# Performance work log

Measured on AMD Instinct MI355X. Metric: run time of the kernel, lower is better.

## Reference

```python
import jax, jax.numpy as jnp
import numpy as np

ATT_HEAD, IN_DIM, OUT_DIM = 4, 256, 64
LEAKY_ALPHA = 0.2
B, N_SRC, N_DST = 4, 2048, 2048


def setup_inputs() -> dict:
    key = jax.random.key(0)
    ks = jax.random.split(key, 8)
    def xavier(k, shape, fan_in, fan_out):
        lim = float(np.sqrt(6.0 / (fan_in + fan_out)))
        return jax.random.uniform(k, shape, jnp.float32, -lim, lim)
    feat_src = jax.random.normal(ks[0], (B, N_SRC, IN_DIM), jnp.float32)
    feat_dst = jax.random.normal(ks[1], (B, N_DST, IN_DIM), jnp.float32)
    W = xavier(ks[2], (ATT_HEAD, IN_DIM, OUT_DIM), IN_DIM, OUT_DIM)
    b = jnp.zeros((OUT_DIM,), jnp.float32)
    w_src = xavier(ks[3], (ATT_HEAD, OUT_DIM), OUT_DIM, 1)
    w_dst = xavier(ks[4], (ATT_HEAD, OUT_DIM), OUT_DIM, 1)
    # nn.Linear(in_dim, in_dim) with xavier_normal_ weight, default-init bias
    std = float(np.sqrt(2.0 / (IN_DIM + IN_DIM)))
    H_w = jax.random.normal(ks[5], (IN_DIM, IN_DIM), jnp.float32) * std
    lim_b = float(1.0 / np.sqrt(IN_DIM))
    H_b = jax.random.uniform(ks[6], (IN_DIM,), jnp.float32, -lim_b, lim_b)
    return {"feat_src": feat_src, "feat_dst": feat_dst, "W": W, "b": b,
            "w_src": w_src, "w_dst": w_dst, "H_w": H_w, "H_b": H_b}


def reference(feat_src, feat_dst, W, b, w_src, w_dst, H_w, H_b):
    # Projections: [B, H, N, out_dim]
    h_src = jnp.einsum('bni,hio->bhno', feat_src, W)
    h_dst = jnp.einsum('bmi,hio->bhmo', feat_dst, W)
    # Additive attention logits
    a_src = jnp.einsum('bhno,ho->bhn', jnp.tanh(h_src), w_src)  # [B,H,N_src]
    a_dst = jnp.einsum('bhmo,ho->bhm', jnp.tanh(h_dst), w_dst)  # [B,H,N_dst]
    attn = a_src[..., :, None] + a_dst[..., None, :]            # [B,H,N_src,N_dst]
    attn = jax.nn.leaky_relu(attn, LEAKY_ALPHA)
    attn = jax.nn.softmax(attn, axis=-1)
    # Weighted sum over dst nodes
    feat_out = jnp.einsum('bhnm,bhmo->bhno', attn, h_dst) + b   # [B,H,N_src,out]
    B_, H_, N_, O_ = feat_out.shape
    feat_out = jnp.transpose(feat_out, (0, 2, 1, 3)).reshape(B_, N_, H_ * O_)
    feat_out = jax.nn.elu(feat_out)
    gate = jax.nn.sigmoid(feat_src @ H_w.T + H_b)
    out = gate * feat_out + (1.0 - gate) * feat_src
    # dropout is identity in eval mode
    return out
```

## Files before the change

### kernel.cpp

```cpp
#include <hip/hip_runtime.h>
#include <math.h>

typedef unsigned int uint32;
typedef __attribute__((ext_vector_type(8))) short bf16x8;
typedef __attribute__((ext_vector_type(4))) float f32x4;

#define BB 4
#define HH 4
#define NSRC 2048
#define NDST 2048
#define IND 256
#define OUTD 64
#define ALPHA 0.2f
#define NB 2048
#define NCH 256

#define OFF_HDST   0
#define OFF_ASRC   2097152
#define OFF_ADST   2129920
#define OFF_PK     2162688
#define OFF_C1     2293760
#define OFF_C2     2555904
#define OFF_CZ1    2818048
#define OFF_CZ2    2822144
#define OFF_T1     2826240
#define OFF_TZ1    2827264
#define OFF_TZ2    2827280
#define OFF_BST    2827296
#define OFF_MM     2860080
#define OFF_GFH    2860112
#define OFF_GFL    2892880

__device__ __forceinline__ float fast_tanh(float x) {
    float e = __expf(2.f * x);
    return 1.f - 2.f / (e + 1.f);
}

__device__ __forceinline__ uint32 f32_to_bf16_rne(float x) {
    uint32 u = __float_as_uint(x);
    return (u + 0x7fffu + ((u >> 16) & 1u)) >> 16;
}

__device__ __forceinline__ void split8(const float* x, bf16x8& h8, bf16x8& l8) {
    uint32 hw[4], lw[4];
    #pragma unroll
    for (int p = 0; p < 4; ++p) {
        uint32 h0 = f32_to_bf16_rne(x[2 * p]);
        float f0 = __uint_as_float(h0 << 16);
        uint32 l0 = f32_to_bf16_rne(x[2 * p] - f0);
        uint32 h1 = f32_to_bf16_rne(x[2 * p + 1]);
        float f1 = __uint_as_float(h1 << 16);
        uint32 l1 = f32_to_bf16_rne(x[2 * p + 1] - f1);
        hw[p] = h0 | (h1 << 16);
        lw[p] = l0 | (l1 << 16);
    }
    h8 = *(bf16x8*)hw; l8 = *(bf16x8*)lw;
}

__global__ __launch_bounds__(256) void k1_mfma(const float* __restrict__ feat_src,
                                               const float* __restrict__ feat_dst,
                                               const float* __restrict__ W,
                                               const float* __restrict__ w_src,
                                               const float* __restrict__ w_dst,
                                               float* __restrict__ ws) {
    __shared__ __align__(16) unsigned short Ahi[32 * 256];
    __shared__ __align__(16) unsigned short Alo[32 * 256];
    int bid = blockIdx.x;
    int t = bid & 63, b = (bid >> 6) & 3, s = bid >> 8;
    int tid = threadIdx.x;
    const float* feat = s ? feat_dst : feat_src;
    const float4* fb = (const float4*)(feat + ((size_t)b * 2048 + t * 32) * IND);
    #pragma unroll
    for (int it = 0; it < 8; ++it) {
        int f4 = it * 256 + tid;
        int row = f4 >> 6, c4 = f4 & 63;
        float4 v = fb[f4];
        float xs[4] = {v.x, v.y, v.z, v.w};
        uint32 hb[4], lb[4];
        #pragma unroll
        for (int j = 0; j < 4; ++j) {
            hb[j] = f32_to_bf16_rne(xs[j]);
            float hf = __uint_as_float(hb[j] << 16);
            lb[j] = f32_to_bf16_rne(xs[j] - hf);
        }
        uint2 hw, lw;
        hw.x = hb[0] | (hb[1] << 16); hw.y = hb[2] | (hb[3] << 16);
        lw.x = lb[0] | (lb[1] << 16); lw.y = lb[2] | (lb[3] << 16);
        int baddr = (row * 512 + c4 * 8) ^ ((row & 7) << 4);
        *(uint2*)((char*)Ahi + baddr) = hw;
        *(uint2*)((char*)Alo + baddr) = lw;
    }
    __syncthreads();
    int w = tid >> 6, l = tid & 63;
    int lr = l & 15, lq = l >> 4;
    const float* Wh = W + (size_t)w * 16384;
    f32x4 acc[2][4];
    #pragma unroll
    for (int mi = 0; mi < 2; ++mi)
        #pragma unroll
        for (int ni = 0; ni < 4; ++ni) acc[mi][ni] = (f32x4)0.f;
    for (int ks = 0; ks < 8; ++ks) {
        bf16x8 ah[2], al[2], bh8[4], bl8[4];
        #pragma unroll
        for (int mi = 0; mi < 2; ++mi) {
            int row = mi * 16 + lr;
            int baddr = (row * 512 + ks * 64 + lq * 16) ^ ((row & 7) << 4);
            ah[mi] = *(const bf16x8*)((const char*)Ahi + baddr);
            al[mi] = *(const bf16x8*)((const char*)Alo + baddr);
        }
        int kb = ks * 32 + lq * 8;
        #pragma unroll
        for (int ni = 0; ni < 4; ++ni) {
            const float* wp = Wh + (size_t)kb * 64 + ni * 16 + lr;
            float xv[8];
            #pragma unroll
            for (int j = 0; j < 8; ++j) xv[j] = wp[j * 64];
            split8(xv, bh8[ni], bl8[ni]);
        }
        #pragma unroll
        for (int mi = 0; mi < 2; ++mi)
            #pragma unroll
            for (int ni = 0; ni < 4; ++ni) {
                acc[mi][ni] = __builtin_amdgcn_mfma_f32_16x16x32_bf16(ah[mi], bh8[ni], acc[mi][ni], 0, 0, 0);
                acc[mi][ni] = __builtin_amdgcn_mfma_f32_16x16x32_bf16(ah[mi], bl8[ni], acc[mi][ni], 0, 0, 0);
                acc[mi][ni] = __builtin_amdgcn_mfma_f32_16x16x32_bf16(al[mi], bh8[ni], acc[mi][ni], 0, 0, 0);
            }
    }
    if (s) {
        float* hd = ws + OFF_HDST + ((size_t)(b * HH + w) * NDST + t * 32) * OUTD;
        #pragma unroll
        for (int mi = 0; mi < 2; ++mi)
            #pragma unroll
            for (int ni = 0; ni < 4; ++ni)
                #pragma unroll
                for (int r = 0; r < 4; ++r)
                    hd[(mi * 16 + lq * 4 + r) * 64 + ni * 16 + lr] = acc[mi][ni][r];
    }
    const float* wa = (s ? w_dst : w_src) + w * OUTD;
    float wa_v[4];
    #pragma unroll
    for (int ni = 0; ni < 4; ++ni) wa_v[ni] = wa[ni * 16 + lr];
    float* ap = ws + (s ? OFF_ADST : OFF_ASRC) + (b * HH + w) * NSRC + t * 32;
    #pragma unroll
    for (int mi = 0; mi < 2; ++mi)
        #pragma unroll
        for (int r = 0; r < 4; ++r) {
            float p = 0.f;
            #pragma unroll
            for (int ni = 0; ni < 4; ++ni) p += fast_tanh(acc[mi][ni][r]) * wa_v[ni];
            p += __shfl_xor(p, 1); p += __shfl_xor(p, 2);
            p += __shfl_xor(p, 4); p += __shfl_xor(p, 8);
            if (lr == 0) ap[mi * 16 + lq * 4 + r] = p;
        }
}

__global__ __launch_bounds__(1024) void kmid(const float* __restrict__ Hw,
                                             float* __restrict__ ws) {
    if (blockIdx.x >= 16) {
        int g = (blockIdx.x - 16) * 1024 + threadIdx.x;
        int l = g & 63, ni = (g >> 6) & 3, ks = (g >> 8) & 7, cb = g >> 11;
        int col = cb * 64 + ni * 16 + (l & 15);
        int k0 = ks * 32 + (l >> 4) * 8;
        unsigned short hs[8], lsv[8];
        #pragma unroll
        for (int j = 0; j < 8; ++j) {
            float w = Hw[(size_t)col * 256 + k0 + j];
            uint32 hb = f32_to_bf16_rne(w);
            float hf = __uint_as_float(hb << 16);
            uint32 lb = f32_to_bf16_rne(w - hf);
            hs[j] = (unsigned short)hb; lsv[j] = (unsigned short)lb;
        }
        unsigned short* fh = (unsigned short*)(ws + OFF_GFH);
        unsigned short* fl = (unsigned short*)(ws + OFF_GFL);
        int slab = ((cb * 8 + ks) * 4 + ni) * 512 + l * 8;
        #pragma unroll
        for (int j = 0; j < 8; ++j) { fh[slab + j] = hs[j]; fl[slab + j] = lsv[j]; }
        return;
    }
    __shared__ int   hist[2048];
    __shared__ float keysP[2048];
    __shared__ int   idxP[2048];
    __shared__ float w1L[2048];
    __shared__ float w2L[2048];
    __shared__ float ST1[16 * 64], ST2[16 * 64];
    __shared__ float SZ1[16], SZ2[16];
    __shared__ float red[32];
    __shared__ float loinv[2];
    __shared__ int wtot[16];
    int bh = blockIdx.x, tid = threadIdx.x;
    int lane = tid & 63, wv = tid >> 6;
    const float* ad = ws + OFF_ADST + bh * NDST;
    float d0 = ad[tid], d1 = ad[tid + 1024];
    float mn = fminf(d0, d1), mx = fmaxf(d0, d1);
    #pragma unroll
    for (int off = 32; off; off >>= 1) {
        mn = fminf(mn, __shfl_xor(mn, off));
        mx = fmaxf(mx, __shfl_xor(mx, off));
    }
    if (lane == 0) { red[wv] = mn; red[16 + wv] = mx; }
    hist[tid] = 0; hist[tid + 1024] = 0;
    __syncthreads();
    if (tid == 0) {
        float lo = red[0], hi = red[16];
        #pragma unroll
        for (int i = 1; i < 16; ++i) { lo = fminf(lo, red[i]); hi = fmaxf(hi, red[16 + i]); }
        float wd = hi - lo;
        float inv = (float)NB / (wd + wd * 1e-6f + 1e-30f);
        loinv[0] = lo; loinv[1] = inv;
        ws[OFF_MM + bh * 2] = lo; ws[OFF_MM + bh * 2 + 1] = inv;
    }
    __syncthreads();
    float lo = loinv[0], inv = loinv[1];
    int b0 = (int)((d0 - lo) * inv); b0 = b0 < 0 ? 0 : (b0 > NB - 1 ? NB - 1 : b0);
    int b1 = (int)((d1 - lo) * inv); b1 = b1 < 0 ? 0 : (b1 > NB - 1 ? NB - 1 : b1);
    atomicAdd(&hist[b0], 1);
    atomicAdd(&hist[b1], 1);
    __syncthreads();
    int h0 = hist[2 * tid], h1 = hist[2 * tid + 1];
    int s = h0 + h1, sc = s;
    #pragma unroll
    for (int off = 1; off < 64; off <<= 1) {
        int v = __shfl_up(sc, off);
        if (lane >= off) sc += v;
    }
    if (lane == 63) wtot[wv] = sc;
    __syncthreads();
    if (tid == 0) {
        int r = 0;
        #pragma unroll
        for (int i = 0; i < 16; ++i) { int v = wtot[i]; wtot[i] = r; r += v; }
    }
    __syncthreads();
    int base = wtot[wv] + (sc - s);
    int* bstg = (int*)(ws + OFF_BST) + bh * (NB + 1);
    hist[2 * tid] = base;
    hist[2 * tid + 1] = base + h0;
    bstg[2 * tid] = base;
    bstg[2 * tid + 1] = base + h0;
    if (tid == 0) bstg[NB] = NDST;
    __syncthreads();
    int p0 = atomicAdd(&hist[b0], 1);
    keysP[p0] = d0; idxP[p0] = tid;
    w1L[p0] = __expf(d0); w2L[p0] = __expf(ALPHA * d0);
    int p1 = atomicAdd(&hist[b1], 1);
    keysP[p1] = d1; idxP[p1] = tid + 1024;
    w1L[p1] = __expf(d1); w2L[p1] = __expf(ALPHA * d1);
    __syncthreads();
    {
        float4* pkg = (float4*)(ws + OFF_PK) + (size_t)bh * 2048;
        pkg[tid] = make_float4(keysP[tid], w1L[tid], w2L[tid],
                               __int_as_float(idxP[tid] * 64));
        pkg[tid + 1024] = make_float4(keysP[tid + 1024], w1L[tid + 1024], w2L[tid + 1024],
                                      __int_as_float(idxP[tid + 1024] * 64));
    }
    const float* hd = ws + OFF_HDST + (size_t)bh * NDST * OUTD;
    float* C1g = ws + OFF_C1 + (size_t)bh * NCH * 64;
    float* C2g = ws + OFF_C2 + (size_t)bh * NCH * 64;
    float* CZ1g = ws + OFF_CZ1 + bh * NCH;
    float* CZ2g = ws + OFF_CZ2 + bh * NCH;
    int o = lane;
    float run1 = 0.f, run2 = 0.f, rz1 = 0.f, rz2 = 0.f;
    for (int k = 0; k < 16; ++k) {
        int c = wv * 16 + k;
        float c1 = 0.f, c2 = 0.f, cz1 = 0.f, cz2 = 0.f;
        #pragma unroll
        for (int ii = 0; ii < 8; ++ii) {
            int i = c * 8 + ii;
            int m = idxP[i];
            float w1 = w1L[i], w2 = w2L[i];
            float hv = hd[m * 64 + o];
            c1 += w1 * hv; c2 += w2 * hv; cz1 += w1; cz2 += w2;
        }
        C1g[c * 64 + o] = c1; C2g[c * 64 + o] = c2;
        if (o == 0) { CZ1g[c] = cz1; CZ2g[c] = cz2; }
        run1 += c1; run2 += c2; rz1 += cz1; rz2 += cz2;
    }
    ST1[wv * 64 + o] = run1; ST2[wv * 64 + o] = run2;
    if (lane == 0) { SZ1[wv] = rz1; SZ2[wv] = rz2; }
    __syncthreads();
    float base1 = 0.f, base2 = 0.f, zb1 = 0.f, zb2 = 0.f;
    for (int ss = 0; ss < wv; ++ss) {
        base1 += ST1[ss * 64 + o]; base2 += ST2[ss * 64 + o];
        zb1 += SZ1[ss];            zb2 += SZ2[ss];
    }
    if (wv == 15) {
        ws[OFF_T1 + bh * 64 + o] = base1 + run1;
        if (o == 0) { ws[OFF_TZ1 + bh] = zb1 + rz1; ws[OFF_TZ2 + bh] = zb2 + rz2; }
    }
    float a1 = base1, a2 = base2, az1 = zb1, az2 = zb2;
    for (int k = 0; k < 16; ++k) {
        int c = wv * 16 + k;
        float v1 = C1g[c * 64 + o]; C1g[c * 64 + o] = a1; a1 += v1;
        float v2 = C2g[c * 64 + o]; C2g[c * 64 + o] = a2; a2 += v2;
        if (o == 0) {
            float vz1 = CZ1g[c]; CZ1g[c] = az1; az1 += vz1;
            float vz2 = CZ2g[c]; CZ2g[c] = az2; az2 += vz2;
        }
    }
}

#define FSTR 260
__global__ __launch_bounds__(512) void k34(const float* __restrict__ feat_src,
                                           const float* __restrict__ Hb,
                                           const float* __restrict__ bias,
                                           const float* __restrict__ ws,
                                           float* __restrict__ out) {
    __shared__ float FOUT[16 * FSTR];
    __shared__ __align__(16) unsigned short Ahi[16 * 256];
    __shared__ __align__(16) unsigned short Alo[16 * 256];
    int bid = blockIdx.x;
    int b = bid >> 7, brow = (bid & 127) * 16;
    int tid = threadIdx.x;
    int o = tid & 63;
    int wv = __builtin_amdgcn_readfirstlane(tid >> 6);
    const float4* fb = (const float4*)(feat_src + ((size_t)b * 2048 + brow) * IND);
    #pragma unroll
    for (int it = 0; it < 2; ++it) {
        int f4 = it * 512 + tid;
        int row = f4 >> 6, c4 = f4 & 63;
        float4 v = fb[f4];
        float xs[4] = {v.x, v.y, v.z, v.w};
        uint32 hb[4], lb[4];
        #pragma unroll
        for (int j = 0; j < 4; ++j) {
            hb[j] = f32_to_bf16_rne(xs[j]);
            float hf = __uint_as_float(hb[j] << 16);
            lb[j] = f32_to_bf16_rne(xs[j] - hf);
        }
        uint2 hw, lw;
        hw.x = hb[0] | (hb[1] << 16); hw.y = hb[2] | (hb[3] << 16);
        lw.x = lb[0] | (lb[1] << 16); lw.y = lb[2] | (lb[3] << 16);
        int baddr = (row * 512 + c4 * 8) ^ ((row & 7) << 4);
        *(uint2*)((char*)Ahi + baddr) = hw;
        *(uint2*)((char*)Alo + baddr) = lw;
    }
    {
        int h = wv >> 1;
        int bh = b * 4 + h;
        int nbase = (wv & 1) * 8;
        float T1v = ws[OFF_T1 + bh * 64 + o];
        float tz1 = ws[OFF_TZ1 + bh], tz2 = ws[OFF_TZ2 + bh];
        float blo = ws[OFF_MM + bh * 2], binv = ws[OFF_MM + bh * 2 + 1];
        float biasv = bias[o];
        int r_l = o & 7;
        float t_l = ws[OFF_ASRC + bh * 2048 + brow + nbase + r_l];
        float th_l = -t_l;
        int bk = (int)floorf((th_l - blo) * binv);
        bk = bk < 0 ? 0 : (bk > NB - 1 ? NB - 1 : bk);
        const int* bst = (const int*)(ws + OFF_BST) + bh * (NB + 1);
        int jstart = bst[bk], jend = bst[bk + 1];
        int cch = (jstart + 4) >> 3; if (cch > NCH - 1) cch = NCH - 1;
        int i0c_l = cch << 3;
        int lo2_l = i0c_l < jstart ? i0c_l : jstart;
        int hi2_l = i0c_l > jend ? i0c_l : jend;
        float czp1_l = ws[OFF_CZ1 + bh * NCH + cch];
        float czp2_l = ws[OFF_CZ2 + bh * NCH + cch];
        float c1v[8], c2v[8];
        #pragma unroll
        for (int r = 0; r < 8; ++r) {
            int cch_r = __builtin_amdgcn_readfirstlane(__shfl(cch, r));
            c1v[r] = ws[OFF_C1 + ((size_t)bh * NCH + cch_r) * 64 + o];
            c2v[r] = ws[OFF_C2 + ((size_t)bh * NCH + cch_r) * 64 + o];
        }
        const float4* pk = (const float4*)(ws + OFF_PK) + (size_t)bh * 2048;
        const float* hd = ws + OFF_HDST + (size_t)bh * NDST * OUTD;
        #pragma unroll
        for (int r = 0; r < 8; ++r) {
            float t_r = __uint_as_float(
                __builtin_amdgcn_readfirstlane(__float_as_uint(__shfl(t_l, r))));
            float th = -t_r;
            int i0c = __builtin_amdgcn_readfirstlane(__shfl(i0c_l, r));
            int lo2 = __builtin_amdgcn_readfirstlane(__shfl(lo2_l, r));
            int hi2 = __builtin_amdgcn_readfirstlane(__shfl(hi2_l, r));
            float p1 = c1v[r], p2 = c2v[r];
            float zp1 = __shfl(czp1_l, r), zp2 = __shfl(czp2_l, r);
            for (int i = lo2; i < hi2; i += 8) {
                float4 q[8];
                #pragma unroll
                for (int j = 0; j < 8; ++j) {
                    int ii = i + j < hi2 ? i + j : hi2 - 1;
                    q[j] = pk[ii];
                }
                float hv[8];
                #pragma unroll
                for (int j = 0; j < 8; ++j)
                    hv[j] = hd[__float_as_int(q[j].w) + o];
                #pragma unroll
                for (int j = 0; j < 8; ++j) {
                    float sel = (q[j].x <= th ? 1.f : 0.f) - (i + j < i0c ? 1.f : 0.f);
                    sel = (i + j < hi2) ? sel : 0.f;
                    float w1 = q[j].y * sel, w2 = q[j].z * sel;
                    p1 += w1 * hv[j]; p2 += w2 * hv[j]; zp1 += w1; zp2 += w2;
                }
            }
            float et = __expf(t_r), et2 = __expf(ALPHA * t_r);
            float num = et * (T1v - p1) + et2 * p2;
            float den = et * (tz1 - zp1) + et2 * zp2;
            FOUT[(nbase + r) * FSTR + h * 64 + o] = num / den + biasv;
        }
    }
    __syncthreads();
    int l = tid & 63;
    int lr = l & 15, lq = l >> 4;
    int cb = wv >> 1, nb = (wv & 1) * 2;
    const uint4* gfh = (const uint4*)(ws + OFF_GFH);
    const uint4* gfl = (const uint4*)(ws + OFF_GFL);
    f32x4 acc[2];
    acc[0] = (f32x4)0.f; acc[1] = (f32x4)0.f;
    for (int ks = 0; ks < 8; ++ks) {
        bf16x8 ah, al, bh8[2], bl8[2];
        {
            int row = lr;
            int baddr = (row * 512 + ks * 64 + lq * 16) ^ ((row & 7) << 4);
            ah = *(const bf16x8*)((const char*)Ahi + baddr);
            al = *(const bf16x8*)((const char*)Alo + baddr);
        }
        #pragma unroll
        for (int ni = 0; ni < 2; ++ni) {
            int idx = ((cb * 8 + ks) * 4 + nb + ni) * 64 + l;
            uint4 th_ = gfh[idx], tl_ = gfl[idx];
            bh8[ni] = *(const bf16x8*)&th_;
            bl8[ni] = *(const bf16x8*)&tl_;
        }
        #pragma unroll
        for (int ni = 0; ni < 2; ++ni) {
            acc[ni] = __builtin_amdgcn_mfma_f32_16x16x32_bf16(ah, bh8[ni], acc[ni], 0, 0, 0);
            acc[ni] = __builtin_amdgcn_mfma_f32_16x16x32_bf16(ah, bl8[ni], acc[ni], 0, 0, 0);
            acc[ni] = __builtin_amdgcn_mfma_f32_16x16x32_bf16(al, bh8[ni], acc[ni], 0, 0, 0);
        }
    }
    #pragma unroll
    for (int ni = 0; ni < 2; ++ni) {
        int c = cb * 64 + (nb + ni) * 16 + lr;
        float hbv = Hb[c];
        #pragma unroll
        for (int r = 0; r < 4; ++r) {
            int rl = lq * 4 + r;
            size_t rg = (size_t)b * 2048 + brow + rl;
            float x = acc[ni][r] + hbv;
            float g = 1.f / (1.f + __expf(-x));
            float fo = FOUT[rl * FSTR + c];
            float e = fo > 0.f ? fo : expm1f(fo);
            float fs = feat_src[rg * 256 + c];
            out[rg * 256 + c] = g * e + (1.f - g) * fs;
        }
    }
}

extern "C" void kernel_launch(void* const* d_in, const int* in_sizes, int n_in,
                              void* d_out, int out_size, void* d_ws, size_t ws_size,
                              hipStream_t stream) {
    const float* feat_src = (const float*)d_in[0];
    const float* feat_dst = (const float*)d_in[1];
    const float* W        = (const float*)d_in[2];
    const float* bias     = (const float*)d_in[3];
    const float* w_src    = (const float*)d_in[4];
    const float* w_dst    = (const float*)d_in[5];
    const float* Hw       = (const float*)d_in[6];
    const float* Hb       = (const float*)d_in[7];
    float* out = (float*)d_out;
    float* ws  = (float*)d_ws;

    k1_mfma<<<512, 256, 0, stream>>>(feat_src, feat_dst, W, w_src, w_dst, ws);
    kmid<<<24, 1024, 0, stream>>>(Hw, ws);
    k34<<<512, 512, 0, stream>>>(feat_src, Hb, bias, ws, out);
}
```

Baseline: 66.96 us.

## Fuse three kernels into one persistent cooperative kernel with grid syncs

Replaces the three separate launches (projection, dst sort/prefix, output+gate) with a single cooperative persistent kernel. Phases are separated by grid-wide syncs, and blocks loop over tiles. The projection phase now uses 512-thread blocks that split output columns across wave halves and reduce partial logits through shared memory. The intent is to remove launch gaps and inter-kernel drain. In exchange, the middle phase runs on only 24 blocks while the rest of the grid waits at the barrier, and occupancy is capped by the cooperative launch.

Measured after the change: 248.2 us. 3.71x slower.

```diff
diff --git a/kernel.cpp b/kernel.cpp
--- a/kernel.cpp
+++ b/kernel.cpp
@@ -1,5 +1,8 @@
 #include <hip/hip_runtime.h>
+#include <hip/hip_cooperative_groups.h>
 #include <math.h>
+
+namespace cg = cooperative_groups;
 
 typedef unsigned int uint32;
 typedef __attribute__((ext_vector_type(8))) short bf16x8;
@@ -57,392 +60,442 @@
     h8 = *(bf16x8*)hw; l8 = *(bf16x8*)lw;
 }
 
-__global__ __launch_bounds__(256) void k1_mfma(const float* __restrict__ feat_src,
-                                               const float* __restrict__ feat_dst,
-                                               const float* __restrict__ W,
-                                               const float* __restrict__ w_src,
-                                               const float* __restrict__ w_dst,
-                                               float* __restrict__ ws) {
-    __shared__ __align__(16) unsigned short Ahi[32 * 256];
-    __shared__ __align__(16) unsigned short Alo[32 * 256];
-    int bid = blockIdx.x;
-    int t = bid & 63, b = (bid >> 6) & 3, s = bid >> 8;
-    int tid = threadIdx.x;
-    const float* feat = s ? feat_dst : feat_src;
-    const float4* fb = (const float4*)(feat + ((size_t)b * 2048 + t * 32) * IND);
-    #pragma unroll
-    for (int it = 0; it < 8; ++it) {
-        int f4 = it * 256 + tid;
-        int row = f4 >> 6, c4 = f4 & 63;
-        float4 v = fb[f4];
-        float xs[4] = {v.x, v.y, v.z, v.w};
-        uint32 hb[4], lb[4];
+#define FSTR 260
+#define SMEM_BYTES 45312
+
+__global__ __launch_bounds__(512, 4) void fused_all(
+        const float* __restrict__ feat_src, const float* __restrict__ feat_dst,
+        const float* __restrict__ W, const float* __restrict__ w_src,
+        const float* __restrict__ w_dst, const float* __restrict__ Hw,
+        const float* __restrict__ Hb, const float* __restrict__ bias,
+        float* __restrict__ ws, float* __restrict__ out) {
+    cg::grid_group gg = cg::this_grid();
+    __shared__ __align__(16) char smem[SMEM_BYTES];
+    const int tid = threadIdx.x;
+    const int nblk = gridDim.x;
+    const int lane = tid & 63, wv = tid >> 6;
+
+    {
+        unsigned short* Ahi = (unsigned short*)smem;
+        unsigned short* Alo = (unsigned short*)(smem + 16384);
+        float* APART = (float*)(smem + 32768);
+        int hh = wv & 3, half = wv >> 2, nb = half * 2;
+        int lr = lane & 15, lq = lane >> 4;
+        const float* Wh = W + (size_t)hh * 16384;
+        for (int tile = blockIdx.x; tile < 512; tile += nblk) {
+            __syncthreads();
+            int t = tile & 63, b = (tile >> 6) & 3, s = tile >> 8;
+            const float* feat = s ? feat_dst : feat_src;
+            const float4* fb = (const float4*)(feat + ((size_t)b * 2048 + t * 32) * IND);
+            #pragma unroll
+            for (int it = 0; it < 4; ++it) {
+                int f4 = it * 512 + tid;
+                int row = f4 >> 6, c4 = f4 & 63;
+                float4 v = fb[f4];
+                float xs[4] = {v.x, v.y, v.z, v.w};
+                uint32 hb[4], lb[4];
+                #pragma unroll
+                for (int j = 0; j < 4; ++j) {
+                    hb[j] = f32_to_bf16_rne(xs[j]);
+                    float hf = __uint_as_float(hb[j] << 16);
+                    lb[j] = f32_to_bf16_rne(xs[j] - hf);
+                }
+                uint2 hw, lw;
+                hw.x = hb[0] | (hb[1] << 16); hw.y = hb[2] | (hb[3] << 16);
+                lw.x = lb[0] | (lb[1] << 16); lw.y = lb[2] | (lb[3] << 16);
+                int baddr = (row * 512 + c4 * 8) ^ ((row & 7) << 4);
+                *(uint2*)((char*)Ahi + baddr) = hw;
+                *(uint2*)((char*)Alo + baddr) = lw;
+            }
+            __syncthreads();
+            f32x4 acc[2][2];
+            #pragma unroll
+            for (int mi = 0; mi < 2; ++mi)
+                #pragma unroll
+                for (int ni = 0; ni < 2; ++ni) acc[mi][ni] = (f32x4)0.f;
+            for (int ks = 0; ks < 8; ++ks) {
+                bf16x8 ah[2], al[2], bh8[2], bl8[2];
+                #pragma unroll
+                for (int mi = 0; mi < 2; ++mi) {
+                    int row = mi * 16 + lr;
+                    int baddr = (row * 512 + ks * 64 + lq * 16) ^ ((row & 7) << 4);
+                    ah[mi] = *(const bf16x8*)((const char*)Ahi + baddr);
+                    al[mi] = *(const bf16x8*)((const char*)Alo + baddr);
+                }
+                int kb = ks * 32 + lq * 8;
+                #pragma unroll
+                for (int ni = 0; ni < 2; ++ni) {
+                    const float* wp = Wh + (size_t)kb * 64 + (nb + ni) * 16 + lr;
+                    float xv[8];
+                    #pragma unroll
+                    for (int j = 0; j < 8; ++j) xv[j] = wp[j * 64];
+                    split8(xv, bh8[ni], bl8[ni]);
+                }
+                #pragma unroll
+                for (int mi = 0; mi < 2; ++mi)
+                    #pragma unroll
+                    for (int ni = 0; ni < 2; ++ni) {
+                        acc[mi][ni] = __builtin_amdgcn_mfma_f32_16x16x32_bf16(ah[mi], bh8[ni], acc[mi][ni], 0, 0, 0);
+                        acc[mi][ni] = __builtin_amdgcn_mfma_f32_16x16x32_bf16(ah[mi], bl8[ni], acc[mi][ni], 0, 0, 0);
+                        acc[mi][ni] = __builtin_amdgcn_mfma_f32_16x16x32_bf16(al[mi], bh8[ni], acc[mi][ni], 0, 0, 0);
+                    }
+            }
+            if (s) {
+                float* hd = ws + OFF_HDST + ((size_t)(b * HH + hh) * NDST + t * 32) * OUTD;
+                #pragma unroll
+                for (int mi = 0; mi < 2; ++mi)
+                    #pragma unroll
+                    for (int ni = 0; ni < 2; ++ni)
+                        #pragma unroll
+                        for (int r = 0; r < 4; ++r)
+                            hd[(mi * 16 + lq * 4 + r) * 64 + (nb + ni) * 16 + lr] = acc[mi][ni][r];
+            }
+            const float* wa = (s ? w_dst : w_src) + hh * OUTD;
+            float wa_v[2];
+            #pragma unroll
+            for (int ni = 0; ni < 2; ++ni) wa_v[ni] = wa[(nb + ni) * 16 + lr];
+            #pragma unroll
+            for (int mi = 0; mi < 2; ++mi)
+                #pragma unroll
+                for (int r = 0; r < 4; ++r) {
+                    float p = fast_tanh(acc[mi][0][r]) * wa_v[0]
+                            + fast_tanh(acc[mi][1][r]) * wa_v[1];
+                    p += __shfl_xor(p, 1); p += __shfl_xor(p, 2);
+                    p += __shfl_xor(p, 4); p += __shfl_xor(p, 8);
+                    if (lr == 0) APART[half * 128 + hh * 32 + mi * 16 + lq * 4 + r] = p;
+                }
+            __syncthreads();
+            if (tid < 128) {
+                int hh2 = tid >> 5, row = tid & 31;
+                float a = APART[hh2 * 32 + row] + APART[128 + hh2 * 32 + row];
+                ws[(s ? OFF_ADST : OFF_ASRC) + (b * HH + hh2) * NSRC + t * 32 + row] = a;
+            }
+        }
+    }
+    __threadfence();
+    gg.sync();
+
+    for (int wb = blockIdx.x; wb < 24; wb += nblk) {
+        __syncthreads();
+        if (wb >= 16) {
+            #pragma unroll
+            for (int q = 0; q < 2; ++q) {
+                int g = (wb - 16) * 1024 + q * 512 + tid;
+                int l = g & 63, ni = (g >> 6) & 3, ks = (g >> 8) & 7, cb = g >> 11;
+                int col = cb * 64 + ni * 16 + (l & 15);
+                int k0 = ks * 32 + (l >> 4) * 8;
+                unsigned short hs[8], lsv[8];
+                #pragma unroll
+                for (int j = 0; j < 8; ++j) {
+                    float w = Hw[(size_t)col * 256 + k0 + j];
+                    uint32 hb = f32_to_bf16_rne(w);
+                    float hf = __uint_as_float(hb << 16);
+                    uint32 lb = f32_to_bf16_rne(w - hf);
+                    hs[j] = (unsigned short)hb; lsv[j] = (unsigned short)lb;
+                }
+                unsigned short* fh = (unsigned short*)(ws + OFF_GFH);
+                unsigned short* fl = (unsigned short*)(ws + OFF_GFL);
+                int slab = ((cb * 8 + ks) * 4 + ni) * 512 + l * 8;
+                #pragma unroll
+                for (int j = 0; j < 8; ++j) { fh[slab + j] = hs[j]; fl[slab + j] = lsv[j]; }
+            }
+            continue;
+        }
+        int bh = wb;
+        int* hist = (int*)smem;
+        float* keysP = (float*)(smem + 8192);
+        int* idxP = (int*)(smem + 16384);
+        float* w1L = (float*)(smem + 24576);
+        float* w2L = (float*)(smem + 32768);
+        float* ST1 = (float*)(smem + 40960);
+        float* ST2 = (float*)(smem + 43008);
+        float* SZ1 = (float*)(smem + 45056);
+        float* SZ2 = (float*)(smem + 45088);
+        float* red = (float*)(smem + 45120);
+        float* loinv = (float*)(smem + 45184);
+        int* wtot = (int*)(smem + 45192);
+        const float* ad = ws + OFF_ADST + bh * NDST;
+        float d0 = ad[tid], d1 = ad[tid + 512], d2 = ad[tid + 1024], d3 = ad[tid + 1536];
+        float mn = fminf(fminf(d0, d1), fminf(d2, d3));
+        float mx = fmaxf(fmaxf(d0, d1), fmaxf(d2, d3));
         #pragma unroll
-        for (int j = 0; j < 4; ++j) {
-            hb[j] = f32_to_bf16_rne(xs[j]);
-            float hf = __uint_as_float(hb[j] << 16);
-            lb[j] = f32_to_bf16_rne(xs[j] - hf);
-        }
-        uint2 hw, lw;
-        hw.x = hb[0] | (hb[1] << 16); hw.y = hb[2] | (hb[3] << 16);
-        lw.x = lb[0] | (lb[1] << 16); lw.y = lb[2] | (lb[3] << 16);
-        int baddr = (row * 512 + c4 * 8) ^ ((row & 7) << 4);
-        *(uint2*)((char*)Ahi + baddr) = hw;
-        *(uint2*)((char*)Alo + baddr) = lw;
+        for (int off = 32; off; off >>= 1) {
+            mn = fminf(mn, __shfl_xor(mn, off));
+            mx = fmaxf(mx, __shfl_xor(mx, off));
+        }
+        if (lane == 0) { red[wv] = mn; red[8 + wv] = mx; }
+        hist[tid] = 0; hist[tid + 512] = 0; hist[tid + 1024] = 0; hist[tid + 1536] = 0;
+        __syncthreads();
+        if (tid == 0) {
+            float lo = red[0], hi = red[8];
+            #pragma unroll
+            for (int i = 1; i < 8; ++i) { lo = fminf(lo, red[i]); hi = fmaxf(hi, red[8 + i]); }
+            float wd = hi - lo;
+            float inv = (float)NB / (wd + wd * 1e-6f + 1e-30f);
+            loinv[0] = lo; loinv[1] = inv;
+            ws[OFF_MM + bh * 2] = lo; ws[OFF_MM + bh * 2 + 1] = inv;
+        }
+        __syncthreads();
+        float lo = loinv[0], inv = loinv[1];
+        int bk0 = (int)((d0 - lo) * inv); bk0 = bk0 < 0 ? 0 : (bk0 > NB - 1 ? NB - 1 : bk0);
+        int bk1 = (int)((d1 - lo) * inv); bk1 = bk1 < 0 ? 0 : (bk1 > NB - 1 ? NB - 1 : bk1);
+        int bk2 = (int)((d2 - lo) * inv); bk2 = bk2 < 0 ? 0 : (bk2 > NB - 1 ? NB - 1 : bk2);
+        int bk3 = (int)((d3 - lo) * inv); bk3 = bk3 < 0 ? 0 : (bk3 > NB - 1 ? NB - 1 : bk3);
+        atomicAdd(&hist[bk0], 1); atomicAdd(&hist[bk1], 1);
+        atomicAdd(&hist[bk2], 1); atomicAdd(&hist[bk3], 1);
+        __syncthreads();
+        int h0 = hist[4 * tid], h1 = hist[4 * tid + 1], h2 = hist[4 * tid + 2], h3 = hist[4 * tid + 3];
+        int s = h0 + h1 + h2 + h3, sc = s;
+        #pragma unroll
+        for (int off = 1; off < 64; off <<= 1) {
+            int v = __shfl_up(sc, off);
+            if (lane >= off) sc += v;
+        }
+        if (lane == 63) wtot[wv] = sc;
+        __syncthreads();
+        if (tid == 0) {
+            int r = 0;
+            #pragma unroll
+            for (int i = 0; i < 8; ++i) { int v = wtot[i]; wtot[i] = r; r += v; }
+        }
+        __syncthreads();
+        int base = wtot[wv] + (sc - s);
+        int* bstg = (int*)(ws + OFF_BST) + bh * (NB + 1);
+        hist[4 * tid] = base;                    bstg[4 * tid] = base;
+        hist[4 * tid + 1] = base + h0;           bstg[4 * tid + 1] = base + h0;
+        hist[4 * tid + 2] = base + h0 + h1;      bstg[4 * tid + 2] = base + h0 + h1;
+        hist[4 * tid + 3] = base + h0 + h1 + h2; bstg[4 * tid + 3] = base + h0 + h1 + h2;
+        if (tid == 0) bstg[NB] = NDST;
+        __syncthreads();
+        {
+            int p = atomicAdd(&hist[bk0], 1);
+            keysP[p] = d0; idxP[p] = tid;
+            w1L[p] = __expf(d0); w2L[p] = __expf(ALPHA * d0);
+            p = atomicAdd(&hist[bk1], 1);
+            keysP[p] = d1; idxP[p] = tid + 512;
+            w1L[p] = __expf(d1); w2L[p] = __expf(ALPHA * d1);
+            p = atomicAdd(&hist[bk2], 1);
+            keysP[p] = d2; idxP[p] = tid + 1024;
+            w1L[p] = __expf(d2); w2L[p] = __expf(ALPHA * d2);
+            p = atomicAdd(&hist[bk3], 1);
+            keysP[p] = d3; idxP[p] = tid + 1536;
+            w1L[p] = __expf(d3); w2L[p] = __expf(ALPHA * d3);
+        }
+        __syncthreads();
+        {
+            float4* pkg = (float4*)(ws + OFF_PK) + (size_t)bh * 2048;
+            #pragma unroll
+            for (int j = 0; j < 4; ++j) {
+                int i = tid + j * 512;
+                pkg[i] = make_float4(keysP[i], w1L[i], w2L[i], __int_as_float(idxP[i] * 64));
+            }
+        }
+        const float* hd = ws + OFF_HDST + (size_t)bh * NDST * OUTD;
+        float* C1g = ws + OFF_C1 + (size_t)bh * NCH * 64;
+        float* C2g = ws + OFF_C2 + (size_t)bh * NCH * 64;
+        float* CZ1g = ws + OFF_CZ1 + bh * NCH;
+        float* CZ2g = ws + OFF_CZ2 + bh * NCH;
+        int o = lane;
+        float run1 = 0.f, run2 = 0.f, rz1 = 0.f, rz2 = 0.f;
+        for (int k = 0; k < 32; ++k) {
+            int c = wv * 32 + k;
+            float c1 = 0.f, c2 = 0.f, cz1 = 0.f, cz2 = 0.f;
+            #pragma unroll
+            for (int ii = 0; ii < 8; ++ii) {
+                int i = c * 8 + ii;
+                int m = idxP[i];
+                float w1 = w1L[i], w2 = w2L[i];
+                float hv = hd[m * 64 + o];
+                c1 += w1 * hv; c2 += w2 * hv; cz1 += w1; cz2 += w2;
+            }
+            C1g[c * 64 + o] = c1; C2g[c * 64 + o] = c2;
+            if (o == 0) { CZ1g[c] = cz1; CZ2g[c] = cz2; }
+            run1 += c1; run2 += c2; rz1 += cz1; rz2 += cz2;
+        }
+        ST1[wv * 64 + o] = run1; ST2[wv * 64 + o] = run2;
+        if (lane == 0) { SZ1[wv] = rz1; SZ2[wv] = rz2; }
+        __syncthreads();
+        float base1 = 0.f, base2 = 0.f, zb1 = 0.f, zb2 = 0.f;
+        for (int ss = 0; ss < wv; ++ss) {
+            base1 += ST1[ss * 64 + o]; base2 += ST2[ss * 64 + o];
+            zb1 += SZ1[ss];            zb2 += SZ2[ss];
+        }
+        if (wv == 7) {
+            ws[OFF_T1 + bh * 64 + o] = base1 + run1;
+            if (o == 0) { ws[OFF_TZ1 + bh] = zb1 + rz1; ws[OFF_TZ2 + bh] = zb2 + rz2; }
+        }
+        float a1 = base1, a2 = base2, az1 = zb1, az2 = zb2;
+        for (int k0 = 0; k0 < 32; k0 += 8) {
+            float v1[8], v2[8];
+            #pragma unroll
+            for (int j = 0; j < 8; ++j) {
+                int c = wv * 32 + k0 + j;
+                v1[j] = C1g[c * 64 + o]; v2[j] = C2g[c * 64 + o];
+            }
+            #pragma unroll
+            for (int j = 0; j < 8; ++j) {
+                int c = wv * 32 + k0 + j;
+                C1g[c * 64 + o] = a1; a1 += v1[j];
+                C2g[c * 64 + o] = a2; a2 += v2[j];
+            }
+            if (o == 0) {
+                float vz1[8], vz2[8];
+                #pragma unroll
+                for (int j = 0; j < 8; ++j) {
+                    int c = wv * 32 + k0 + j;
+                    vz1[j] = CZ1g[c]; vz2[j] = CZ2g[c];
+                }
+                #pragma unroll
+                for (int j = 0; j < 8; ++j) {
+                    int c = wv * 32 + k0 + j;
+                    CZ1g[c] = az1; az1 += vz1[j];
+                    CZ2g[c] = az2; az2 += vz2[j];
+                }
+            }
+        }
     }
-    __syncthreads();
-    int w = tid >> 6, l = tid & 63;
-    int lr = l & 15, lq = l >> 4;
-    const float* Wh = W + (size_t)w * 16384;
-    f32x4 acc[2][4];
-    #pragma unroll
-    for (int mi = 0; mi < 2; ++mi)
-        #pragma unroll
-        for (int ni = 0; ni < 4; ++ni) acc[mi][ni] = (f32x4)0.f;
-    for (int ks = 0; ks < 8; ++ks) {
-        bf16x8 ah[2], al[2], bh8[4], bl8[4];
-        #pragma unroll
-        for (int mi = 0; mi < 2; ++mi) {
-            int row = mi * 16 + lr;
-            int baddr = (row * 512 + ks * 64 + lq * 16) ^ ((row & 7) << 4);
-            ah[mi] = *(const bf16x8*)((const char*)Ahi + baddr);
-            al[mi] = *(const bf16x8*)((const char*)Alo + baddr);
-        }
-        int kb = ks * 32 + lq * 8;
-        #pragma unroll
-        for (int ni = 0; ni < 4; ++ni) {
-            const float* wp = Wh + (size_t)kb * 64 + ni * 16 + lr;
-            float xv[8];
-            #pragma unroll
-            for (int j = 0; j < 8; ++j) xv[j] = wp[j * 64];
-            split8(xv, bh8[ni], bl8[ni]);
-        }
-        #pragma unroll
-        for (int mi = 0; mi < 2; ++mi)
-            #pragma unroll
-            for (int ni = 0; ni < 4; ++ni) {
-                acc[mi][ni] = __builtin_amdgcn_mfma_f32_16x16x32_bf16(ah[mi], bh8[ni], acc[mi][ni], 0, 0, 0);
-                acc[mi][ni] = __builtin_amdgcn_mfma_f32_16x16x32_bf16(ah[mi], bl8[ni], acc[mi][ni], 0, 0, 0);
-                acc[mi][ni] = __builtin_amdgcn_mfma_f32_16x16x32_bf16(al[mi], bh8[ni], acc[mi][ni], 0, 0, 0);
-            }
-    }
-    if (s) {
-        float* hd = ws + OFF_HDST + ((size_t)(b * HH + w) * NDST + t * 32) * OUTD;
-        #pragma unroll
-        for (int mi = 0; mi < 2; ++mi)
-            #pragma unroll
-            for (int ni = 0; ni < 4; ++ni)
-                #pragma unroll
-                for (int r = 0; r < 4; ++r)
-                    hd[(mi * 16 + lq * 4 + r) * 64 + ni * 16 + lr] = acc[mi][ni][r];
-    }
-    const float* wa = (s ? w_dst : w_src) + w * OUTD;
-    float wa_v[4];
-    #pragma unroll
-    for (int ni = 0; ni < 4; ++ni) wa_v[ni] = wa[ni * 16 + lr];
-    float* ap = ws + (s ? OFF_ADST : OFF_ASRC) + (b * HH + w) * NSRC + t * 32;
-    #pragma unroll
-    for (int mi = 0; mi < 2; ++mi)
-        #pragma unroll
-        for (int r = 0; r < 4; ++r) {
-            float p = 0.f;
-            #pragma unroll
-            for (int ni = 0; ni < 4; ++ni) p += fast_tanh(acc[mi][ni][r]) * wa_v[ni];
-            p += __shfl_xor(p, 1); p += __shfl_xor(p, 2);
-            p += __shfl_xor(p, 4); p += __shfl_xor(p, 8);
-            if (lr == 0) ap[mi * 16 + lq * 4 + r] = p;
-        }
-}
-
-__global__ __launch_bounds__(1024) void kmid(const float* __restrict__ Hw,
-                                             float* __restrict__ ws) {
-    if (blockIdx.x >= 16) {
-        int g = (blockIdx.x - 16) * 1024 + threadIdx.x;
-        int l = g & 63, ni = (g >> 6) & 3, ks = (g >> 8) & 7, cb = g >> 11;
-        int col = cb * 64 + ni * 16 + (l & 15);
-        int k0 = ks * 32 + (l >> 4) * 8;
-        unsigned short hs[8], lsv[8];
-        #pragma unroll
-        for (int j = 0; j < 8; ++j) {
-            float w = Hw[(size_t)col * 256 + k0 + j];
-            uint32 hb = f32_to_bf16_rne(w);
-            float hf = __uint_as_float(hb << 16);
-            uint32 lb = f32_to_bf16_rne(w - hf);
-            hs[j] = (unsigned short)hb; lsv[j] = (unsigned short)lb;
-        }
-        unsigned short* fh = (unsigned short*)(ws + OFF_GFH);
-        unsigned short* fl = (unsigned short*)(ws + OFF_GFL);
-        int slab = ((cb * 8 + ks) * 4 + ni) * 512 + l * 8;
-        #pragma unroll
-        for (int j = 0; j < 8; ++j) { fh[slab + j] = hs[j]; fl[slab + j] = lsv[j]; }
-        return;
-    }
-    __shared__ int   hist[2048];
-    __shared__ float keysP[2048];
-    __shared__ int   idxP[2048];
-    __shared__ float w1L[2048];
-    __shared__ float w2L[2048];
-    __shared__ float ST1[16 * 64], ST2[16 * 64];
-    __shared__ float SZ1[16], SZ2[16];
-    __shared__ float red[32];
-    __shared__ float loinv[2];
-    __shared__ int wtot[16];
-    int bh = blockIdx.x, tid = threadIdx.x;
-    int lane = tid & 63, wv = tid >> 6;
-    const float* ad = ws + OFF_ADST + bh * NDST;
-    float d0 = ad[tid], d1 = ad[tid + 1024];
-    float mn = fminf(d0, d1), mx = fmaxf(d0, d1);
-    #pragma unroll
-    for (int off = 32; off; off >>= 1) {
-        mn = fminf(mn, __shfl_xor(mn, off));
-        mx = fmaxf(mx, __shfl_xor(mx, off));
-    }
-    if (lane == 0) { red[wv] = mn; red[16 + wv] = mx; }
-    hist[tid] = 0; hist[tid + 1024] = 0;
-    __syncthreads();
-    if (tid == 0) {
-        float lo = red[0], hi = red[16];
-        #pragma unroll
-        for (int i = 1; i < 16; ++i) { lo = fminf(lo, red[i]); hi = fmaxf(hi, red[16 + i]); }
-        float wd = hi - lo;
-        float inv = (float)NB / (wd + wd * 1e-6f + 1e-30f);
-        loinv[0] = lo; loinv[1] = inv;
-        ws[OFF_MM + bh * 2] = lo; ws[OFF_MM + bh * 2 + 1] = inv;
-    }
-    __syncthreads();
-    float lo = loinv[0], inv = loinv[1];
-    int b0 = (int)((d0 - lo) * inv); b0 = b0 < 0 ? 0 : (b0 > NB - 1 ? NB - 1 : b0);
-    int b1 = (int)((d1 - lo) * inv); b1 = b1 < 0 ? 0 : (b1 > NB - 1 ? NB - 1 : b1);
-    atomicAdd(&hist[b0], 1);
-    atomicAdd(&hist[b1], 1);
-    __syncthreads();
-    int h0 = hist[2 * tid], h1 = hist[2 * tid + 1];
-    int s = h0 + h1, sc = s;
-    #pragma unroll
-    for (int off = 1; off < 64; off <<= 1) {
-        int v = __shfl_up(sc, off);
-        if (lane >= off) sc += v;
-    }
-    if (lane == 63) wtot[wv] = sc;
-    __syncthreads();
-    if (tid == 0) {
-        int r = 0;
-        #pragma unroll
-        for (int i = 0; i < 16; ++i) { int v = wtot[i]; wtot[i] = r; r += v; }
-    }
-    __syncthreads();
-    int base = wtot[wv] + (sc - s);
-    int* bstg = (int*)(ws + OFF_BST) + bh * (NB + 1);
-    hist[2 * tid] = base;
-    hist[2 * tid + 1] = base + h0;
-    bstg[2 * tid] = base;
-    bstg[2 * tid + 1] = base + h0;
-    if (tid == 0) bstg[NB] = NDST;
-    __syncthreads();
-    int p0 = atomicAdd(&hist[b0], 1);
-    keysP[p0] = d0; idxP[p0] = tid;
-    w1L[p0] = __expf(d0); w2L[p0] = __expf(ALPHA * d0);
-    int p1 = atomicAdd(&hist[b1], 1);
-    keysP[p1] = d1; idxP[p1] = tid + 1024;
-    w1L[p1] = __expf(d1); w2L[p1] = __expf(ALPHA * d1);
-    __syncthreads();
+    __threadfence();
+    gg.sync();
+
     {
-        float4* pkg = (float4*)(ws + OFF_PK) + (size_t)bh * 2048;
-        pkg[tid] = make_float4(keysP[tid], w1L[tid], w2L[tid],
-                               __int_as_float(idxP[tid] * 64));
-        pkg[tid + 1024] = make_float4(keysP[tid + 1024], w1L[tid + 1024], w2L[tid + 1024],
-                                      __int_as_float(idxP[tid + 1024] * 64));
-    }
-    const float* hd = ws + OFF_HDST + (size_t)bh * NDST * OUTD;
-    float* C1g = ws + OFF_C1 + (size_t)bh * NCH * 64;
-    float* C2g = ws + OFF_C2 + (size_t)bh * NCH * 64;
-    float* CZ1g = ws + OFF_CZ1 + bh * NCH;
-    float* CZ2g = ws + OFF_CZ2 + bh * NCH;
-    int o = lane;
-    float run1 = 0.f, run2 = 0.f, rz1 = 0.f, rz2 = 0.f;
-    for (int k = 0; k < 16; ++k) {
-        int c = wv * 16 + k;
-        float c1 = 0.f, c2 = 0.f, cz1 = 0.f, cz2 = 0.f;
-        #pragma unroll
-        for (int ii = 0; ii < 8; ++ii) {
-            int i = c * 8 + ii;
-            int m = idxP[i];
-            float w1 = w1L[i], w2 = w2L[i];
-            float hv = hd[m * 64 + o];
-            c1 += w1 * hv; c2 += w2 * hv; cz1 += w1; cz2 += w2;
-        }
-        C1g[c * 64 + o] = c1; C2g[c * 64 + o] = c2;
-        if (o == 0) { CZ1g[c] = cz1; CZ2g[c] = cz2; }
-        run1 += c1; run2 += c2; rz1 += cz1; rz2 += cz2;
-    }
-    ST1[wv * 64 + o] = run1; ST2[wv * 64 + o] = run2;
-    if (lane == 0) { SZ1[wv] = rz1; SZ2[wv] = rz2; }
-    __syncthreads();
-    float base1 = 0.f, base2 = 0.f, zb1 = 0.f, zb2 = 0.f;
-    for (int ss = 0; ss < wv; ++ss) {
-        base1 += ST1[ss * 64 + o]; base2 += ST2[ss * 64 + o];
-        zb1 += SZ1[ss];            zb2 += SZ2[ss];
-    }
-    if (wv == 15) {
-        ws[OFF_T1 + bh * 64 + o] = base1 + run1;
-        if (o == 0) { ws[OFF_TZ1 + bh] = zb1 + rz1; ws[OFF_TZ2 + bh] = zb2 + rz2; }
-    }
-    float a1 = base1, a2 = base2, az1 = zb1, az2 = zb2;
-    for (int k = 0; k < 16; ++k) {
-        int c = wv * 16 + k;
-        float v1 = C1g[c * 64 + o]; C1g[c * 64 + o] = a1; a1 += v1;
-        float v2 = C2g[c * 64 + o]; C2g[c * 64 + o] = a2; a2 += v2;
-        if (o == 0) {
-            float vz1 = CZ1g[c]; CZ1g[c] = az1; az1 += vz1;
-            float vz2 = CZ2g[c]; CZ2g[c] = az2; az2 += vz2;
-        }
-    }
-}
-
-#define FSTR 260
-__global__ __launch_bounds__(512) void k34(const float* __restrict__ feat_src,
-                                           const float* __restrict__ Hb,
-                                           const float* __restrict__ bias,
-                                           const float* __restrict__ ws,
-                                           float* __restrict__ out) {
-    __shared__ float FOUT[16 * FSTR];
-    __shared__ __align__(16) unsigned short Ahi[16 * 256];
-    __shared__ __align__(16) unsigned short Alo[16 * 256];
-    int bid = blockIdx.x;
-    int b = bid >> 7, brow = (bid & 127) * 16;
-    int tid = threadIdx.x;
-    int o = tid & 63;
-    int wv = __builtin_amdgcn_readfirstlane(tid >> 6);
-    const float4* fb = (const float4*)(feat_src + ((size_t)b * 2048 + brow) * IND);
-    #pragma unroll
-    for (int it = 0; it < 2; ++it) {
-        int f4 = it * 512 + tid;
-        int row = f4 >> 6, c4 = f4 & 63;
-        float4 v = fb[f4];
-        float xs[4] = {v.x, v.y, v.z, v.w};
-        uint32 hb[4], lb[4];
-        #pragma unroll
-        for (int j = 0; j < 4; ++j) {
-            hb[j] = f32_to_bf16_rne(xs[j]);
-            float hf = __uint_as_float(hb[j] << 16);
-            lb[j] = f32_to_bf16_rne(xs[j] - hf);
-        }
-        uint2 hw, lw;
-        hw.x = hb[0] | (hb[1] << 16); hw.y = hb[2] | (hb[3] << 16);
-        lw.x = lb[0] | (lb[1] << 16); lw.y = lb[2] | (lb[3] << 16);
-        int baddr = (row * 512 + c4 * 8) ^ ((row & 7) << 4);
-        *(uint2*)((char*)Ahi + baddr) = hw;
-        *(uint2*)((char*)Alo + baddr) = lw;
-    }
-    {
-        int h = wv >> 1;
-        int bh = b * 4 + h;
-        int nbase = (wv & 1) * 8;
-        float T1v = ws[OFF_T1 + bh * 64 + o];
-        float tz1 = ws[OFF_TZ1 + bh], tz2 = ws[OFF_TZ2 + bh];
-        float blo = ws[OFF_MM + bh * 2], binv = ws[OFF_MM + bh * 2 + 1];
-        float biasv = bias[o];
-        int r_l = o & 7;
-        float t_l = ws[OFF_ASRC + bh * 2048 + brow + nbase + r_l];
-        float th_l = -t_l;
-        int bk = (int)floorf((th_l - blo) * binv);
-        bk = bk < 0 ? 0 : (bk > NB - 1 ? NB - 1 : bk);
-        const int* bst = (const int*)(ws + OFF_BST) + bh * (NB + 1);
-        int jstart = bst[bk], jend = bst[bk + 1];
-        int cch = (jstart + 4) >> 3; if (cch > NCH - 1) cch = NCH - 1;
-        int i0c_l = cch << 3;
-        int lo2_l = i0c_l < jstart ? i0c_l : jstart;
-        int hi2_l = i0c_l > jend ? i0c_l : jend;
-        float czp1_l = ws[OFF_CZ1 + bh * NCH + cch];
-        float czp2_l = ws[OFF_CZ2 + bh * NCH + cch];
-        float c1v[8], c2v[8];
-        #pragma unroll
-        for (int r = 0; r < 8; ++r) {
-            int cch_r = __builtin_amdgcn_readfirstlane(__shfl(cch, r));
-            c1v[r] = ws[OFF_C1 + ((size_t)bh * NCH + cch_r) * 64 + o];
-            c2v[r] = ws[OFF_C2 + ((size_t)bh * NCH + cch_r) * 64 + o];
-        }
-        const float4* pk = (const float4*)(ws + OFF_PK) + (size_t)bh * 2048;
-        const float* hd = ws + OFF_HDST + (size_t)bh * NDST * OUTD;
-        #pragma unroll
-        for (int r = 0; r < 8; ++r) {
-            float t_r = __uint_as_float(
-                __builtin_amdgcn_readfirstlane(__float_as_uint(__shfl(t_l, r))));
-            float th = -t_r;
-            int i0c = __builtin_amdgcn_readfirstlane(__shfl(i0c_l, r));
-            int lo2 = __builtin_amdgcn_readfirstlane(__shfl(lo2_l, r));
-            int hi2 = __builtin_amdgcn_readfirstlane(__shfl(hi2_l, r));
-            float p1 = c1v[r], p2 = c2v[r];
-            float zp1 = __shfl(czp1_l, r), zp2 = __shfl(czp2_l, r);
-            for (int i = lo2; i < hi2; i += 8) {
-                float4 q[8];
-                #pragma unroll
-                for (int j = 0; j < 8; ++j) {
-                    int ii = i + j < hi2 ? i + j : hi2 - 1;
-                    q[j] = pk[ii];
-                }
-                float hv[8];
-                #pragma unroll
-                for (int j = 0; j < 8; ++j)
-                    hv[j] = hd[__float_as_int(q[j].w) + o];
-                #pragma unroll
-                for (int j = 0; j < 8; ++j) {
-                    float sel = (q[j].x <= th ? 1.f : 0.f) - (i + j < i0c ? 1.f : 0.f);
-                    sel = (i + j < hi2) ? sel : 0.f;
-                    float w1 = q[j].y * sel, w2 = q[j].z * sel;
-                    p1 += w1 * hv[j]; p2 += w2 * hv[j]; zp1 += w1; zp2 += w2;
-                }
-            }
-            float et = __expf(t_r), et2 = __expf(ALPHA * t_r);
-            float num = et * (T1v - p1) + et2 * p2;
-            float den = et * (tz1 - zp1) + et2 * zp2;
-            FOUT[(nbase + r) * FSTR + h * 64 + o] = num / den + biasv;
-        }
-    }
-    __syncthreads();
-    int l = tid & 63;
-    int lr = l & 15, lq = l >> 4;
-    int cb = wv >> 1, nb = (wv & 1) * 2;
-    const uint4* gfh = (const uint4*)(ws + OFF_GFH);
-    const uint4* gfl = (const uint4*)(ws + OFF_GFL);
-    f32x4 acc[2];
-    acc[0] = (f32x4)0.f; acc[1] = (f32x4)0.f;
-    for (int ks = 0; ks < 8; ++ks) {
-        bf16x8 ah, al, bh8[2], bl8[2];
-        {
-            int row = lr;
-            int baddr = (row * 512 + ks * 64 + lq * 16) ^ ((row & 7) << 4);
-            ah = *(const bf16x8*)((const char*)Ahi + baddr);
-            al = *(const bf16x8*)((const char*)Alo + baddr);
-        }
-        #pragma unroll
-        for (int ni = 0; ni < 2; ++ni) {
-            int idx = ((cb * 8 + ks) * 4 + nb + ni) * 64 + l;
-            uint4 th_ = gfh[idx], tl_ = gfl[idx];
-            bh8[ni] = *(const bf16x8*)&th_;
-            bl8[ni] = *(const bf16x8*)&tl_;
-        }
-        #pragma unroll
-        for (int ni = 0; ni < 2; ++ni) {
-            acc[ni] = __builtin_amdgcn_mfma_f32_16x16x32_bf16(ah, bh8[ni], acc[ni], 0, 0, 0);
-            acc[ni] = __builtin_amdgcn_mfma_f32_16x16x32_bf16(ah, bl8[ni], acc[ni], 0, 0, 0);
-            acc[ni] = __builtin_amdgcn_mfma_f32_16x16x32_bf16(al, bh8[ni], acc[ni], 0, 0, 0);
-        }
-    }
-    #pragma unroll
-    for (int ni = 0; ni < 2; ++ni) {
-        int c = cb * 64 + (nb + ni) * 16 + lr;
-        float hbv = Hb[c];
-        #pragma unroll
-        for (int r = 0; r < 4; ++r) {
-            int rl = lq * 4 + r;
-            size_t rg = (size_t)b * 2048 + brow + rl;
-            float x = acc[ni][r] + hbv;
-            float g = 1.f / (1.f + __expf(-x));
-            float fo = FOUT[rl * FSTR + c];
-            float e = fo > 0.f ? fo : expm1f(fo);
-            float fs = feat_src[rg * 256 + c];
-            out[rg * 256 + c] = g * e + (1.f - g) * fs;
+        float* FOUT = (float*)smem;
+        unsigned short* Ahi = (unsigned short*)(smem + 16640);
+        unsigned short* Alo = (unsigned short*)(smem + 24832);
+        int o = lane;
+        for (int tile = blockIdx.x; tile < 512; tile += nblk) {
+            __syncthreads();
+            int b = tile >> 7, brow = (tile & 127) * 16;
+            const float4* fb = (const float4*)(feat_src + ((size_t)b * 2048 + brow) * IND);
+            #pragma unroll
+            for (int it = 0; it < 2; ++it) {
+                int f4 = it * 512 + tid;
+                int row = f4 >> 6, c4 = f4 & 63;
+                float4 v = fb[f4];
+                float xs[4] = {v.x, v.y, v.z, v.w};
+                uint32 hb[4], lb[4];
+                #pragma unroll
+                for (int j = 0; j < 4; ++j) {
+                    hb[j] = f32_to_bf16_rne(xs[j]);
+                    float hf = __uint_as_float(hb[j] << 16);
+                    lb[j] = f32_to_bf16_rne(xs[j] - hf);
+                }
+                uint2 hw, lw;
+                hw.x = hb[0] | (hb[1] << 16); hw.y = hb[2] | (hb[3] << 16);
+                lw.x = lb[0] | (lb[1] << 16); lw.y = lb[2] | (lb[3] << 16);
+                int baddr = (row * 512 + c4 * 8) ^ ((row & 7) << 4);
+                *(uint2*)((char*)Ahi + baddr) = hw;
+                *(uint2*)((char*)Alo + baddr) = lw;
+            }
+            {
+                int h = wv >> 1;
+                int bh = b * 4 + h;
+                int nbase = (wv & 1) * 8;
+                float T1v = ws[OFF_T1 + bh * 64 + o];
+                float tz1 = ws[OFF_TZ1 + bh], tz2 = ws[OFF_TZ2 + bh];
+                float blo = ws[OFF_MM + bh * 2], binv = ws[OFF_MM + bh * 2 + 1];
+                float biasv = bias[o];
+                int r_l = o & 7;
+                float t_l = ws[OFF_ASRC + bh * 2048 + brow + nbase + r_l];
+                float th_l = -t_l;
+                int bk = (int)floorf((th_l - blo) * binv);
+                bk = bk < 0 ? 0 : (bk > NB - 1 ? NB - 1 : bk);
+                const int* bst = (const int*)(ws + OFF_BST) + bh * (NB + 1);
+                int jstart = bst[bk], jend = bst[bk + 1];
+                int cch = (jstart + 4) >> 3; if (cch > NCH - 1) cch = NCH - 1;
+                int i0c_l = cch << 3;
+                int lo2_l = i0c_l < jstart ? i0c_l : jstart;
+                int hi2_l = i0c_l > jend ? i0c_l : jend;
+                float czp1_l = ws[OFF_CZ1 + bh * NCH + cch];
+                float czp2_l = ws[OFF_CZ2 + bh * NCH + cch];
+                float c1v[8], c2v[8];
+                #pragma unroll
+                for (int r = 0; r < 8; ++r) {
+                    int cch_r = __builtin_amdgcn_readfirstlane(__shfl(cch, r));
+                    c1v[r] = ws[OFF_C1 + ((size_t)bh * NCH + cch_r) * 64 + o];
+                    c2v[r] = ws[OFF_C2 + ((size_t)bh * NCH + cch_r) * 64 + o];
+                }
+                const float4* pk = (const float4*)(ws + OFF_PK) + (size_t)bh * 2048;
+                const float* hd = ws + OFF_HDST + (size_t)bh * NDST * OUTD;
+                #pragma unroll
+                for (int r = 0; r < 8; ++r) {
+                    float t_r = __uint_as_float(
+                        __builtin_amdgcn_readfirstlane(__float_as_uint(__shfl(t_l, r))));
+                    float th = -t_r;
+                    int i0c = __builtin_amdgcn_readfirstlane(__shfl(i0c_l, r));
+                    int lo2 = __builtin_amdgcn_readfirstlane(__shfl(lo2_l, r));
+                    int hi2 = __builtin_amdgcn_readfirstlane(__shfl(hi2_l, r));
+                    float p1 = c1v[r], p2 = c2v[r];
+                    float zp1 = __shfl(czp1_l, r), zp2 = __shfl(czp2_l, r);
+                    for (int i = lo2; i < hi2; i += 8) {
+                        float4 q[8];
+                        #pragma unroll
+                        for (int j = 0; j < 8; ++j) {
+                            int ii = i + j < hi2 ? i + j : hi2 - 1;
+                            q[j] = pk[ii];
+                        }
+                        float hv[8];
+                        #pragma unroll
+                        for (int j = 0; j < 8; ++j)
+                            hv[j] = hd[__float_as_int(q[j].w) + o];
+                        #pragma unroll
+                        for (int j = 0; j < 8; ++j) {
+                            float sel = (q[j].x <= th ? 1.f : 0.f) - (i + j < i0c ? 1.f : 0.f);
+                            sel = (i + j < hi2) ? sel : 0.f;
+                            float w1 = q[j].y * sel, w2 = q[j].z * sel;
+                            p1 += w1 * hv[j]; p2 += w2 * hv[j]; zp1 += w1; zp2 += w2;
+                        }
+                    }
+                    float et = __expf(t_r), et2 = __expf(ALPHA * t_r);
+                    float num = et * (T1v - p1) + et2 * p2;
+                    float den = et * (tz1 - zp1) + et2 * zp2;
+                    FOUT[(nbase + r) * FSTR + h * 64 + o] = num / den + biasv;
+                }
+            }
+            __syncthreads();
+            int lr = lane & 15, lq = lane >> 4;
+            int cb = wv >> 1, nb = (wv & 1) * 2;
+            const uint4* gfh = (const uint4*)(ws + OFF_GFH);
+            const uint4* gfl = (const uint4*)(ws + OFF_GFL);
+            f32x4 acc[2];
+            acc[0] = (f32x4)0.f; acc[1] = (f32x4)0.f;
+            for (int ks = 0; ks < 8; ++ks) {
+                bf16x8 ah, al, bh8[2], bl8[2];
+                {
+                    int row = lr;
+                    int baddr = (row * 512 + ks * 64 + lq * 16) ^ ((row & 7) << 4);
+                    ah = *(const bf16x8*)((const char*)Ahi + baddr);
+                    al = *(const bf16x8*)((const char*)Alo + baddr);
+                }
+                #pragma unroll
+                for (int ni = 0; ni < 2; ++ni) {
+                    int idx = ((cb * 8 + ks) * 4 + nb + ni) * 64 + lane;
+                    uint4 th_ = gfh[idx], tl_ = gfl[idx];
+                    bh8[ni] = *(const bf16x8*)&th_;
+                    bl8[ni] = *(const bf16x8*)&tl_;
+                }
+                #pragma unroll
+                for (int ni = 0; ni < 2; ++ni) {
+                    acc[ni] = __builtin_amdgcn_mfma_f32_16x16x32_bf16(ah, bh8[ni], acc[ni], 0, 0, 0);
+                    acc[ni] = __builtin_amdgcn_mfma_f32_16x16x32_bf16(ah, bl8[ni], acc[ni], 0, 0, 0);
+                    acc[ni] = __builtin_amdgcn_mfma_f32_16x16x32_bf16(al, bh8[ni], acc[ni], 0, 0, 0);
+                }
+            }
+            #pragma unroll
+            for (int ni = 0; ni < 2; ++ni) {
+                int c = cb * 64 + (nb + ni) * 16 + lr;
+                float hbv = Hb[c];
+                #pragma unroll
+                for (int r = 0; r < 4; ++r) {
+                    int rl = lq * 4 + r;
+                    size_t rg = (size_t)b * 2048 + brow + rl;
+                    float x = acc[ni][r] + hbv;
+                    float g = 1.f / (1.f + __expf(-x));
+                    float fo = FOUT[rl * FSTR + c];
+                    float e = fo > 0.f ? fo : expm1f(fo);
+                    float fs = feat_src[rg * 256 + c];
+                    out[rg * 256 + c] = g * e + (1.f - g) * fs;
+                }
+            }
         }
     }
 }
@@ -461,7 +514,15 @@
     float* out = (float*)d_out;
     float* ws  = (float*)d_ws;
 
-    k1_mfma<<<512, 256, 0, stream>>>(feat_src, feat_dst, W, w_src, w_dst, ws);
-    kmid<<<24, 1024, 0, stream>>>(Hw, ws);
-    k34<<<512, 512, 0, stream>>>(feat_src, Hb, bias, ws, out);
+    int maxb = 0;
+    hipOccupancyMaxActiveBlocksPerMultiprocessor(&maxb, fused_all, 512, 0);
+    int grid = maxb * 256;
+    if (grid > 512) grid = 512;
+    if (grid < 1) grid = 1;
+
+    void* args[] = {(void*)&feat_src, (void*)&feat_dst, (void*)&W,
+                    (void*)&w_src, (void*)&w_dst, (void*)&Hw,
+                    (void*)&Hb, (void*)&bias, (void*)&ws, (void*)&out};
+    hipLaunchCooperativeKernel((void*)fused_all, dim3(grid), dim3(512),
+                               args, 0, stream);
 }
```
